# Optimization experiments

Measured on AMD Instinct MI355X. Metric: run time of the kernel, lower is better.

## Reference

```python
import jax, jax.numpy as jnp
import numpy as np

NUM_M = 512
NUM_T = 64
MAX_STEPS = 20
TAU = 1.0


def setup_inputs() -> dict:
    key = jax.random.key(0)
    ks = jax.random.split(key, 10)
    num_m, num_t = NUM_M, NUM_T
    inp = {
        "v_src": jax.random.normal(ks[0], (1, num_m), jnp.float32),
        "v_target": jax.random.normal(ks[1], (1, num_m), jnp.float32),
        # small-magnitude generators so matrix_exp stays well-conditioned
        "omegas": jax.random.normal(ks[2], (num_t, num_m, num_m), jnp.float32) * 0.01,
        "W1": jax.random.normal(ks[3], (2 * num_m, 256), jnp.float32) * (1.0 / np.sqrt(2 * num_m)),
        "b1": jnp.zeros((256,), jnp.float32),
        "W2": jax.random.normal(ks[4], (256, 128), jnp.float32) * (1.0 / np.sqrt(256)),
        "b2": jnp.zeros((128,), jnp.float32),
        "W3": jax.random.normal(ks[5], (128, num_t), jnp.float32) * (1.0 / np.sqrt(128)),
        "b3": jnp.zeros((num_t,), jnp.float32),
        # pre-sampled gumbel noise, one draw per step: [max_steps, B, num_t]
        "gumbel_noise": jax.random.gumbel(ks[6], (MAX_STEPS, 1, num_t), jnp.float32),
    }
    return inp


def reference(v_src, v_target, omegas, W1, b1, W2, b2, W3, b3, gumbel_noise):
    tgt_idx = jnp.argmax(v_target, axis=-1)  # [B]

    def mlp(x):
        h = jax.nn.relu(x @ W1 + b1)
        h = jax.nn.relu(h @ W2 + b2)
        return h @ W3 + b3  # [B, num_t]

    batched_expm = jax.vmap(jax.scipy.linalg.expm)

    def step(carry, g):
        v, done = carry  # v: [B, num_m], done: [B] bool
        x = jnp.concatenate([v, v_target], axis=-1)        # [B, 2*num_m]
        logits = mlp(x)                                     # [B, num_t]
        # gumbel_softmax(tau=1.0, hard=False)
        soft = jax.nn.softmax((logits + g) / TAU, axis=-1)
        omega_k = jnp.einsum('bt,tmk->bmk', soft, omegas)   # [B, m, m]
        R_k = batched_expm(omega_k)                         # [B, m, m]
        v_new = jnp.einsum('bmk,bk->bm', R_k, v)            # [B, m]
        # freeze state and zero-pad logits once the target marking was reached
        v_out = jnp.where(done[:, None], v, v_new)
        logits_out = jnp.where(done[:, None], jnp.zeros_like(logits), logits)
        done_new = done | (jnp.argmax(v_new, axis=-1) == tgt_idx)
        return (v_out, done_new), logits_out

    done0 = jnp.zeros((v_src.shape[0],), bool)
    (v_final, _), logits_seq = jax.lax.scan(step, (v_src, done0), gumbel_noise)
    # logits_seq: [max_steps, B, num_t]; B==1 -> [max_steps, num_t] (torch squeeze(0))
    return v_final, logits_seq[:, 0, :]
```

## Files before the change

### kernel.cpp

```cpp
#include <hip/hip_runtime.h>
#include <hip/hip_fp16.h>


#define NBLK 256
#define NTHR 512
#define NSTEP 20
#define NTAY 3
#define RBUF 4

typedef unsigned long long ull;

#define XW(buf, i) (X + ((buf) << 8) + (i))

__device__ __forceinline__ float wredsum(float p) {
#pragma unroll
  for (int off = 32; off > 0; off >>= 1) p += __shfl_xor(p, off, 64);
  return p;
}

__device__ __forceinline__ void wredsum2(float& p0, float& p1) {
#pragma unroll
  for (int off = 32; off > 0; off >>= 1) {
    float t0 = __shfl_xor(p0, off, 64);
    float t1 = __shfl_xor(p1, off, 64);
    p0 += t0;
    p1 += t1;
  }
}

__device__ __forceinline__ void publish2(ull* w, float v0, float v1, unsigned int tag2) {
  unsigned int u0 = (__float_as_uint(v0) & ~3u) | tag2;
  ull x = (ull)u0 | ((ull)__float_as_uint(v1) << 32);
  __hip_atomic_store(w, x, __ATOMIC_RELAXED, __HIP_MEMORY_SCOPE_AGENT);
}

__device__ __forceinline__ float2 poll2(ull* w, unsigned int tag2) {
  int it = 0;
  for (;;) {
    ull x = __hip_atomic_load(w, __ATOMIC_RELAXED, __HIP_MEMORY_SCOPE_AGENT);
    if ((unsigned int)(x & 3u) == tag2) {
      float2 r;
      r.x = __uint_as_float((unsigned int)x);
      r.y = __uint_as_float((unsigned int)(x >> 32));
      return r;
    }
    if (it == 0)      __builtin_amdgcn_s_sleep(1);
    else if (it == 1) __builtin_amdgcn_s_sleep(2);
    else              __builtin_amdgcn_s_sleep(4);
    if (it < 2) ++it;
  }
}

__device__ __forceinline__ void poll8(ull* w0, unsigned int tg, float* o) {
  ull x0 = 0, x1 = 0, x2 = 0, x3 = 0;
  bool g0 = false, g1 = false, g2 = false, g3 = false;
  int it = 0;
  for (;;) {
    if (!g0) { ull x = __hip_atomic_load(w0,     __ATOMIC_RELAXED, __HIP_MEMORY_SCOPE_AGENT); if ((unsigned int)(x & 3u) == tg) { x0 = x; g0 = true; } }
    if (!g1) { ull x = __hip_atomic_load(w0 + 1, __ATOMIC_RELAXED, __HIP_MEMORY_SCOPE_AGENT); if ((unsigned int)(x & 3u) == tg) { x1 = x; g1 = true; } }
    if (!g2) { ull x = __hip_atomic_load(w0 + 2, __ATOMIC_RELAXED, __HIP_MEMORY_SCOPE_AGENT); if ((unsigned int)(x & 3u) == tg) { x2 = x; g2 = true; } }
    if (!g3) { ull x = __hip_atomic_load(w0 + 3, __ATOMIC_RELAXED, __HIP_MEMORY_SCOPE_AGENT); if ((unsigned int)(x & 3u) == tg) { x3 = x; g3 = true; } }
    if (g0 && g1 && g2 && g3) break;
    if (it == 0)      __builtin_amdgcn_s_sleep(1);
    else if (it == 1) __builtin_amdgcn_s_sleep(2);
    else              __builtin_amdgcn_s_sleep(4);
    if (it < 2) ++it;
  }
  o[0] = __uint_as_float((unsigned int)x0); o[1] = __uint_as_float((unsigned int)(x0 >> 32));
  o[2] = __uint_as_float((unsigned int)x1); o[3] = __uint_as_float((unsigned int)(x1 >> 32));
  o[4] = __uint_as_float((unsigned int)x2); o[5] = __uint_as_float((unsigned int)(x2 >> 32));
  o[6] = __uint_as_float((unsigned int)x3); o[7] = __uint_as_float((unsigned int)(x3 >> 32));
}

__global__ __launch_bounds__(NTHR) void petri_kernel(
    const float* __restrict__ vsrc, const float* __restrict__ vtgt,
    const float* __restrict__ omg,  const float* __restrict__ W1,
    const float* __restrict__ b1,   const float* __restrict__ W2,
    const float* __restrict__ b2,   const float* __restrict__ W3,
    const float* __restrict__ b3,   const float* __restrict__ gum,
    ull* __restrict__ X, float* __restrict__ out) {
  __shared__ __half2 oh[64 * 512];
  __shared__ __align__(16) float A0_s[512];
  __shared__ __align__(16) float A1_s[512];
  __shared__ __align__(16) float v_loc[512];
  __shared__ float tgt_s[512];
  __shared__ float w1c_s[1024];
  __shared__ float gum_s[NSTEP * 64];
  __shared__ float b2_s[128], b3_s[64];
  __shared__ float soft_s[64], h1_s[256], h2_s[128];
  __shared__ float redp[512];
  __shared__ float llog[NSTEP * 64];
  __shared__ float rf8[8];
  __shared__ int   ri8[8];
  __shared__ float cB_s[1];
  __shared__ int   bc[1];

  const int b = blockIdx.x, tid = threadIdx.x;
  const int wv = tid >> 6, ln = tid & 63;

  v_loc[tid] = vsrc[tid];
  tgt_s[tid] = vtgt[tid];
  w1c_s[tid] = W1[tid * 256 + b];
  w1c_s[tid + 512] = W1[(tid + 512) * 256 + b];
  for (int i = tid; i < NSTEP * 64; i += NTHR) gum_s[i] = gum[i];
  if (tid >= NTHR - 128) {
    int j = tid - (NTHR - 128);
    b2_s[j] = b2[j];
    if (j < 64) b3_s[j] = b3[j];
  }
  float w2r[64];
  {
    const int o = tid & 127, q = tid >> 7;
    const float* p = W2 + ((q << 6) * 128) + o;
#pragma unroll
    for (int i = 0; i < 64; ++i) w2r[i] = p[i * 128];
  }
  float w3r[16];
  {
    const int o = tid & 63, q = tid >> 6;
    const float* p = W3 + ((q << 4) * 64) + o;
#pragma unroll
    for (int i = 0; i < 16; ++i) w3r[i] = p[i * 64];
  }
  {
    const int tq = tid >> 7;
    const int c4 = (tid & 127) << 2;
    const float* rp = omg + (b << 10) + c4;
#pragma unroll 4
    for (int g = 0; g < 16; ++g) {
      const int t = (g << 2) + tq;
      const float* p = rp + t * 262144;
      const float4 f0 = *(const float4*)(p);
      const float4 f1 = *(const float4*)(p + 512);
      __half2* dst = oh + t * 512 + c4;
      dst[0] = __floats2half2_rn(f0.x, f1.x);
      dst[1] = __floats2half2_rn(f0.y, f1.y);
      dst[2] = __floats2half2_rn(f0.z, f1.z);
      dst[3] = __floats2half2_rn(f0.w, f1.w);
    }
  }
  __syncthreads();

  {
    float p = tgt_s[tid] * w1c_s[tid + 512];
    p = wredsum(p);
    if (ln == 0) rf8[wv] = p;
    __syncthreads();
    if (tid == 0) {
      float a = b1[b];
      for (int q = 0; q < 8; ++q) a += rf8[q];
      cB_s[0] = a;
    }
    __syncthreads();
  }

  int tgtIdx;
  {
    float v = tgt_s[tid]; int ix = tid;
#pragma unroll
    for (int off = 32; off > 0; off >>= 1) {
      float ov = __shfl_xor(v, off, 64); int oi = __shfl_xor(ix, off, 64);
      if (ov > v || (ov == v && oi < ix)) { v = ov; ix = oi; }
    }
    if (ln == 0) { rf8[wv] = v; ri8[wv] = ix; }
    __syncthreads();
    if (tid == 0) {
      float bv = rf8[0]; int bix = ri8[0];
      for (int q = 1; q < 8; ++q)
        if (rf8[q] > bv || (rf8[q] == bv && ri8[q] < bix)) { bv = rf8[q]; bix = ri8[q]; }
      bc[0] = bix;
    }
    __syncthreads();
    tgtIdx = bc[0];
    __syncthreads();
  }

  float vreg[8], w1t[8];
  if (wv == 0) {
    const int l8 = ln << 3;
#pragma unroll
    for (int k = 0; k < 8; ++k) { vreg[k] = v_loc[l8 + k]; w1t[k] = w1c_s[l8 + k]; }
    float p = 0.f;
#pragma unroll
    for (int k = 0; k < 8; ++k) p = fmaf(vreg[k], w1t[k], p);
    p = wredsum(p);
    if (ln == 0) {
      float h = fmaxf(p + cB_s[0], 0.f);
      publish2(XW(0, b), h, h, 0u);
    }
  }

  int d = 0;
  int nAct = 0;
  int r = 0;

  for (int s = 0; s < NSTEP; ++s) {
    if (d) continue;
    nAct = s + 1;

    {
      const int buf = r & (RBUF - 1);
      const unsigned int tg = (unsigned int)((r >> 2) & 3);
      if (tid < 256) h1_s[tid] = poll2(XW(buf, tid), tg).x;
      __syncthreads();
      ++r;
    }

    {
      const int q = tid >> 7;
      const float* hp = h1_s + (q << 6);
      float a0 = 0.f, a1 = 0.f, a2 = 0.f, a3 = 0.f;
#pragma unroll
      for (int i = 0; i < 64; i += 4) {
        a0 = fmaf(hp[i],     w2r[i],     a0);
        a1 = fmaf(hp[i + 1], w2r[i + 1], a1);
        a2 = fmaf(hp[i + 2], w2r[i + 2], a2);
        a3 = fmaf(hp[i + 3], w2r[i + 3], a3);
      }
      redp[tid] = (a0 + a1) + (a2 + a3);
    }
    __syncthreads();
    if (tid < 128) {
      float rr = redp[tid] + redp[tid + 128] + redp[tid + 256] + redp[tid + 384] + b2_s[tid];
      h2_s[tid] = fmaxf(rr, 0.f);
    }
    __syncthreads();
    {
      const int q = tid >> 6;
      const float* hp = h2_s + (q << 4);
      float a0 = 0.f, a1 = 0.f;
#pragma unroll
      for (int i = 0; i < 16; i += 2) {
        a0 = fmaf(hp[i],     w3r[i],     a0);
        a1 = fmaf(hp[i + 1], w3r[i + 1], a1);
      }
      redp[tid] = a0 + a1;
    }
    __syncthreads();
    if (tid < 64) {
      float a = b3_s[tid];
#pragma unroll
      for (int q = 0; q < 8; ++q) a += redp[tid + (q << 6)];
      float lg = a + gum_s[s * 64 + tid];
      float mx = lg;
#pragma unroll
      for (int off = 32; off > 0; off >>= 1) mx = fmaxf(mx, __shfl_xor(mx, off, 64));
      float e = __expf(lg - mx);
      float sm = e;
#pragma unroll
      for (int off = 32; off > 0; off >>= 1) sm += __shfl_xor(sm, off, 64);
      soft_s[tid] = e / sm;
      llog[s * 64 + tid] = a;
    }
    __syncthreads();

    {
      float a0 = 0.f, a1 = 0.f, c0 = 0.f, c1 = 0.f;
#pragma unroll 8
      for (int t = 0; t < 64; t += 2) {
        float2 xy0 = __half22float2(oh[t * 512 + tid]);
        float2 xy1 = __half22float2(oh[(t + 1) * 512 + tid]);
        float s0 = soft_s[t], s1 = soft_s[t + 1];
        a0 = fmaf(s0, xy0.x, a0);
        c0 = fmaf(s0, xy0.y, c0);
        a1 = fmaf(s1, xy1.x, a1);
        c1 = fmaf(s1, xy1.y, c1);
      }
      A0_s[tid] = a0 + a1;
      A1_s[tid] = c0 + c1;
    }
    __syncthreads();

    if (wv == 0) {
      const int l8 = ln << 3;
      const float4 a00 = *(const float4*)(A0_s + l8);
      const float4 a01 = *(const float4*)(A0_s + l8 + 4);
      const float4 a10 = *(const float4*)(A1_s + l8);
      const float4 a11 = *(const float4*)(A1_s + l8 + 4);
      const float vb0 = v_loc[b << 1], vb1 = v_loc[(b << 1) + 1];
      float wreg[8];
#pragma unroll
      for (int k = 0; k < 8; ++k) wreg[k] = vreg[k];
      float acc0 = 0.f, acc1 = 0.f;
#pragma unroll
      for (int n = 1; n <= NTAY; ++n) {
        const int rr = r + (n - 1);
        const int buf = rr & (RBUF - 1);
        const unsigned int tg = (unsigned int)((rr >> 2) & 3);
        float p0 = 0.f, p1 = 0.f;
        p0 = fmaf(a00.x, wreg[0], p0); p0 = fmaf(a00.y, wreg[1], p0);
        p0 = fmaf(a00.z, wreg[2], p0); p0 = fmaf(a00.w, wreg[3], p0);
        p0 = fmaf(a01.x, wreg[4], p0); p0 = fmaf(a01.y, wreg[5], p0);
        p0 = fmaf(a01.z, wreg[6], p0); p0 = fmaf(a01.w, wreg[7], p0);
        p1 = fmaf(a10.x, wreg[0], p1); p1 = fmaf(a10.y, wreg[1], p1);
        p1 = fmaf(a10.z, wreg[2], p1); p1 = fmaf(a10.w, wreg[3], p1);
        p1 = fmaf(a11.x, wreg[4], p1); p1 = fmaf(a11.y, wreg[5], p1);
        p1 = fmaf(a11.z, wreg[6], p1); p1 = fmaf(a11.w, wreg[7], p1);
        wredsum2(p0, p1);
        if (ln == 0) {
          float s0, s1;
          if (n == 1) {
            s0 = p0; s1 = p1;
            acc0 = vb0 + s0; acc1 = vb1 + s1;
          } else {
            const float inv = (n == 2) ? 0.5f : (1.0f / 3.0f);
            s0 = p0 * inv; s1 = p1 * inv;
            acc0 += s0; acc1 += s1;
          }
          const float q0 = (n < NTAY) ? s0 : acc0;
          const float q1 = (n < NTAY) ? s1 : acc1;
          publish2(XW(buf, b), q0, q1, tg);
        }
        poll8(XW(buf, (ln << 2)), tg, wreg);
      }
      if (s + 1 < NSTEP) {
        const int rh = r + NTAY;
        const unsigned int tgh = (unsigned int)((rh >> 2) & 3);
        float ph = 0.f;
#pragma unroll
        for (int k = 0; k < 8; ++k) ph = fmaf(wreg[k], w1t[k], ph);
        ph = wredsum(ph);
        if (ln == 0) {
          float h = fmaxf(ph + cB_s[0], 0.f);
          publish2(XW(rh & (RBUF - 1), b), h, h, tgh);
        }
      }
#pragma unroll
      for (int k = 0; k < 8; ++k) vreg[k] = wreg[k];
      *(float4*)(v_loc + l8)     = make_float4(wreg[0], wreg[1], wreg[2], wreg[3]);
      *(float4*)(v_loc + l8 + 4) = make_float4(wreg[4], wreg[5], wreg[6], wreg[7]);
      float mv = wreg[0]; int mi = l8;
#pragma unroll
      for (int k = 1; k < 8; ++k) if (wreg[k] > mv) { mv = wreg[k]; mi = l8 + k; }
#pragma unroll
      for (int off = 32; off > 0; off >>= 1) {
        float ov = __shfl_xor(mv, off, 64); int oi = __shfl_xor(mi, off, 64);
        if (ov > mv || (ov == mv && oi < mi)) { mv = ov; mi = oi; }
      }
      if (ln == 0) bc[0] = (mi == tgtIdx) ? 1 : 0;
    }
    __syncthreads();
    if (bc[0]) d = 1;
    r += NTAY;
  }

  if (b == 0) {
    out[tid] = v_loc[tid];
    for (int i = tid; i < NSTEP * 64; i += NTHR)
      out[512 + i] = (i < nAct * 64) ? llog[i] : 0.0f;
  }
}

extern "C" void kernel_launch(void* const* d_in, const int* in_sizes, int n_in,
                              void* d_out, int out_size, void* d_ws, size_t ws_size,
                              hipStream_t stream) {
  (void)in_sizes; (void)n_in; (void)out_size; (void)ws_size;
  petri_kernel<<<dim3(NBLK), dim3(NTHR), 0, stream>>>(
      (const float*)d_in[0], (const float*)d_in[1], (const float*)d_in[2],
      (const float*)d_in[3], (const float*)d_in[4], (const float*)d_in[5],
      (const float*)d_in[6], (const float*)d_in[7], (const float*)d_in[8],
      (const float*)d_in[9], (ull*)d_ws, (float*)d_out);
}
```

Baseline: 381.8 us.

## Compute layer-1 MLP locally per block instead of a cross-block exchange

Each block keeps the whole W1 v-half in registers as half2 and computes all 256 hidden-1 units from its local v, rather than each block computing one unit and publishing it through global memory for every block to poll. This removes one grid-wide publish/poll round per step from the serial dependency chain, at the cost of a fp16 W1 (precision loss), 128 extra registers per thread and more redundant FLOPs. Exchange slots are also padded to 64-byte strides to avoid false sharing, and launch bounds now request 2 blocks per CU.

```diff
diff --git a/kernel.cpp b/kernel.cpp
--- a/kernel.cpp
+++ b/kernel.cpp
@@ -10,13 +10,7 @@
 
 typedef unsigned long long ull;
 
-#define XW(buf, i) (X + ((buf) << 8) + (i))
-
-__device__ __forceinline__ float wredsum(float p) {
-#pragma unroll
-  for (int off = 32; off > 0; off >>= 1) p += __shfl_xor(p, off, 64);
-  return p;
-}
+#define XW(buf, i) (X + ((((buf) << 8) + (i)) << 3))
 
 __device__ __forceinline__ void wredsum2(float& p0, float& p1) {
 #pragma unroll
@@ -56,10 +50,10 @@
   bool g0 = false, g1 = false, g2 = false, g3 = false;
   int it = 0;
   for (;;) {
-    if (!g0) { ull x = __hip_atomic_load(w0,     __ATOMIC_RELAXED, __HIP_MEMORY_SCOPE_AGENT); if ((unsigned int)(x & 3u) == tg) { x0 = x; g0 = true; } }
-    if (!g1) { ull x = __hip_atomic_load(w0 + 1, __ATOMIC_RELAXED, __HIP_MEMORY_SCOPE_AGENT); if ((unsigned int)(x & 3u) == tg) { x1 = x; g1 = true; } }
-    if (!g2) { ull x = __hip_atomic_load(w0 + 2, __ATOMIC_RELAXED, __HIP_MEMORY_SCOPE_AGENT); if ((unsigned int)(x & 3u) == tg) { x2 = x; g2 = true; } }
-    if (!g3) { ull x = __hip_atomic_load(w0 + 3, __ATOMIC_RELAXED, __HIP_MEMORY_SCOPE_AGENT); if ((unsigned int)(x & 3u) == tg) { x3 = x; g3 = true; } }
+    if (!g0) { ull x = __hip_atomic_load(w0,      __ATOMIC_RELAXED, __HIP_MEMORY_SCOPE_AGENT); if ((unsigned int)(x & 3u) == tg) { x0 = x; g0 = true; } }
+    if (!g1) { ull x = __hip_atomic_load(w0 + 8,  __ATOMIC_RELAXED, __HIP_MEMORY_SCOPE_AGENT); if ((unsigned int)(x & 3u) == tg) { x1 = x; g1 = true; } }
+    if (!g2) { ull x = __hip_atomic_load(w0 + 16, __ATOMIC_RELAXED, __HIP_MEMORY_SCOPE_AGENT); if ((unsigned int)(x & 3u) == tg) { x2 = x; g2 = true; } }
+    if (!g3) { ull x = __hip_atomic_load(w0 + 24, __ATOMIC_RELAXED, __HIP_MEMORY_SCOPE_AGENT); if ((unsigned int)(x & 3u) == tg) { x3 = x; g3 = true; } }
     if (g0 && g1 && g2 && g3) break;
     if (it == 0)      __builtin_amdgcn_s_sleep(1);
     else if (it == 1) __builtin_amdgcn_s_sleep(2);
@@ -72,7 +66,7 @@
   o[6] = __uint_as_float((unsigned int)x3); o[7] = __uint_as_float((unsigned int)(x3 >> 32));
 }
 
-__global__ __launch_bounds__(NTHR) void petri_kernel(
+__global__ __launch_bounds__(NTHR, 2) void petri_kernel(
     const float* __restrict__ vsrc, const float* __restrict__ vtgt,
     const float* __restrict__ omg,  const float* __restrict__ W1,
     const float* __restrict__ b1,   const float* __restrict__ W2,
@@ -85,14 +79,14 @@
   __shared__ __align__(16) float v_loc[512];
   __shared__ float tgt_s[512];
   __shared__ float w1c_s[1024];
+  __shared__ float cB_s[256];
   __shared__ float gum_s[NSTEP * 64];
   __shared__ float b2_s[128], b3_s[64];
   __shared__ float soft_s[64], h1_s[256], h2_s[128];
   __shared__ float redp[512];
   __shared__ float llog[NSTEP * 64];
-  __shared__ float rf8[8];
+  __shared__ float rf8[8], rf8b[8];
   __shared__ int   ri8[8];
-  __shared__ float cB_s[1];
   __shared__ int   bc[1];
 
   const int b = blockIdx.x, tid = threadIdx.x;
@@ -121,6 +115,17 @@
     const float* p = W3 + ((q << 4) * 64) + o;
 #pragma unroll
     for (int i = 0; i < 16; ++i) w3r[i] = p[i * 64];
+  }
+  __half2 w1h[128];
+  {
+    const int j = tid & 255, hf = tid >> 8;
+    const float* wp = W1 + ((hf << 8) * 256) + j;
+#pragma unroll
+    for (int i = 0; i < 128; ++i) {
+      const float a = wp[((i << 1)) * 256];
+      const float c = wp[((i << 1) + 1) * 256];
+      w1h[i] = __floats2half2_rn(a, c);
+    }
   }
   {
     const int tq = tid >> 7;
@@ -142,14 +147,20 @@
   __syncthreads();
 
   {
-    float p = tgt_s[tid] * w1c_s[tid + 512];
-    p = wredsum(p);
-    if (ln == 0) rf8[wv] = p;
+    float p0 = tgt_s[tid] * w1c_s[tid + 512];
+    float p1 = v_loc[tid] * w1c_s[tid];
+    wredsum2(p0, p1);
+    if (ln == 0) { rf8[wv] = p0; rf8b[wv] = p1; }
     __syncthreads();
     if (tid == 0) {
-      float a = b1[b];
-      for (int q = 0; q < 8; ++q) a += rf8[q];
-      cB_s[0] = a;
+      float cB = b1[b], dv = 0.f;
+      for (int q = 0; q < 8; ++q) { cB += rf8[q]; dv += rf8b[q]; }
+      publish2(XW(0, b), fmaxf(dv + cB, 0.f), cB, 0u);
+    }
+    if (tid < 256) {
+      float2 g = poll2(XW(0, tid), 0u);
+      h1_s[tid] = g.x;
+      cB_s[tid] = g.y;
     }
     __syncthreads();
   }
@@ -175,36 +186,13 @@
     __syncthreads();
   }
 
-  float vreg[8], w1t[8];
-  if (wv == 0) {
-    const int l8 = ln << 3;
-#pragma unroll
-    for (int k = 0; k < 8; ++k) { vreg[k] = v_loc[l8 + k]; w1t[k] = w1c_s[l8 + k]; }
-    float p = 0.f;
-#pragma unroll
-    for (int k = 0; k < 8; ++k) p = fmaf(vreg[k], w1t[k], p);
-    p = wredsum(p);
-    if (ln == 0) {
-      float h = fmaxf(p + cB_s[0], 0.f);
-      publish2(XW(0, b), h, h, 0u);
-    }
-  }
-
   int d = 0;
   int nAct = 0;
-  int r = 0;
+  int r = 1;
 
   for (int s = 0; s < NSTEP; ++s) {
     if (d) continue;
     nAct = s + 1;
-
-    {
-      const int buf = r & (RBUF - 1);
-      const unsigned int tg = (unsigned int)((r >> 2) & 3);
-      if (tid < 256) h1_s[tid] = poll2(XW(buf, tid), tg).x;
-      __syncthreads();
-      ++r;
-    }
 
     {
       const int q = tid >> 7;
@@ -279,8 +267,12 @@
       const float4 a11 = *(const float4*)(A1_s + l8 + 4);
       const float vb0 = v_loc[b << 1], vb1 = v_loc[(b << 1) + 1];
       float wreg[8];
-#pragma unroll
-      for (int k = 0; k < 8; ++k) wreg[k] = vreg[k];
+      {
+        const float4 v0 = *(const float4*)(v_loc + l8);
+        const float4 v1 = *(const float4*)(v_loc + l8 + 4);
+        wreg[0] = v0.x; wreg[1] = v0.y; wreg[2] = v0.z; wreg[3] = v0.w;
+        wreg[4] = v1.x; wreg[5] = v1.y; wreg[6] = v1.z; wreg[7] = v1.w;
+      }
       float acc0 = 0.f, acc1 = 0.f;
 #pragma unroll
       for (int n = 1; n <= NTAY; ++n) {
@@ -313,20 +305,6 @@
         }
         poll8(XW(buf, (ln << 2)), tg, wreg);
       }
-      if (s + 1 < NSTEP) {
-        const int rh = r + NTAY;
-        const unsigned int tgh = (unsigned int)((rh >> 2) & 3);
-        float ph = 0.f;
-#pragma unroll
-        for (int k = 0; k < 8; ++k) ph = fmaf(wreg[k], w1t[k], ph);
-        ph = wredsum(ph);
-        if (ln == 0) {
-          float h = fmaxf(ph + cB_s[0], 0.f);
-          publish2(XW(rh & (RBUF - 1), b), h, h, tgh);
-        }
-      }
-#pragma unroll
-      for (int k = 0; k < 8; ++k) vreg[k] = wreg[k];
       *(float4*)(v_loc + l8)     = make_float4(wreg[0], wreg[1], wreg[2], wreg[3]);
       *(float4*)(v_loc + l8 + 4) = make_float4(wreg[4], wreg[5], wreg[6], wreg[7]);
       float mv = wreg[0]; int mi = l8;
@@ -340,7 +318,28 @@
       if (ln == 0) bc[0] = (mi == tgtIdx) ? 1 : 0;
     }
     __syncthreads();
-    if (bc[0]) d = 1;
+    if (bc[0]) {
+      d = 1;
+    } else if (s + 1 < NSTEP) {
+      const int hf = tid >> 8;
+      const float4* vp4 = (const float4*)(v_loc + (hf << 8));
+      float acA = 0.f, acB = 0.f, acC = 0.f, acD = 0.f;
+#pragma unroll
+      for (int i = 0; i < 64; ++i) {
+        const float4 v4 = vp4[i];
+        const float2 wa = __half22float2(w1h[2 * i]);
+        const float2 wb = __half22float2(w1h[2 * i + 1]);
+        acA = fmaf(wa.x, v4.x, acA);
+        acB = fmaf(wa.y, v4.y, acB);
+        acC = fmaf(wb.x, v4.z, acC);
+        acD = fmaf(wb.y, v4.w, acD);
+      }
+      redp[tid] = (acA + acB) + (acC + acD);
+      __syncthreads();
+      if (tid < 256)
+        h1_s[tid] = fmaxf(redp[tid] + redp[tid + 256] + cB_s[tid], 0.f);
+      __syncthreads();
+    }
     r += NTAY;
   }
 
```

New measurement: 1.231 ms. +222.6%, slower.
